# Kernel tuning notes

Hardware: AMD Instinct MI355X
Metric: run time of the kernel (lower is better)

The kernel has to match this reference:

```python
import jax, jax.numpy as jnp
import numpy as np

EPS_LN = 1e-5

def layer_norm(x, g, b):
    mu = x.mean(-1, keepdims=True)
    var = ((x - mu) ** 2).mean(-1, keepdims=True)
    return (x - mu) / jnp.sqrt(var + EPS_LN) * g + b

def spike(x):
    # MultiSpike: quantized spike activation, forward = clip(round(x), 0, 4)
    return jnp.clip(jnp.round(x), 0.0, 4.0)

def setup_inputs() -> dict:
    key = jax.random.key(0)
    ks = jax.random.split(key, 8)
    B, C, H, W = 16, 256, 56, 56
    hid = 128
    inp = {}
    inp['feature_map'] = jax.random.normal(ks[0], (B, C, H, W), jnp.float32)
    inp['audio_feature'] = jax.random.normal(ks[1], (B, 1, C), jnp.float32)
    # MINE params
    inp['w1'] = jax.random.normal(ks[2], (hid, 2 * C), jnp.float32) / np.sqrt(2 * C)
    inp['b1'] = jnp.zeros((hid,), jnp.float32)
    inp['g1'] = jnp.ones((hid,), jnp.float32)
    inp['beta1'] = jnp.zeros((hid,), jnp.float32)
    inp['w2'] = jax.random.normal(ks[3], (hid // 2, hid), jnp.float32) / np.sqrt(hid)
    inp['b2'] = jnp.zeros((hid // 2,), jnp.float32)
    inp['g2'] = jnp.ones((hid // 2,), jnp.float32)
    inp['beta2'] = jnp.zeros((hid // 2,), jnp.float32)
    inp['w3'] = jax.random.normal(ks[4], (1, hid // 2), jnp.float32) / np.sqrt(hid // 2)
    inp['b3'] = jnp.zeros((1,), jnp.float32)
    # MI params
    inp['pw'] = jax.random.normal(ks[5], (C, C), jnp.float32) / np.sqrt(C)
    inp['pb'] = jnp.zeros((C,), jnp.float32)
    inp['pg'] = jnp.ones((C,), jnp.float32)
    inp['pbeta'] = jnp.zeros((C,), jnp.float32)
    return inp

def reference(feature_map, audio_feature, w1, b1, g1, beta1, w2, b2, g2, beta2,
              w3, b3, pw, pb, pg, pbeta):
    B, C, H, W = feature_map.shape
    # visual tokens: [B*H*W, C]
    visual = feature_map.transpose(0, 2, 3, 1).reshape(B * H * W, C)
    # broadcast audio to every spatial position: [B*H*W, C]
    audio = jnp.broadcast_to(audio_feature[:, 0][:, None, None, :], (B, H, W, C)).reshape(B * H * W, C)
    # MINE MLP on joint features
    joint = jnp.concatenate([visual, audio], axis=1)            # [BHW, 2C]
    h = spike(layer_norm(joint @ w1.T + b1, g1, beta1))          # [BHW, 128]
    h = spike(layer_norm(h @ w2.T + b2, g2, beta2))              # [BHW, 64]
    mi = (h @ w3.T + b3)[:, 0]                                   # [BHW]
    mi_map = mi.reshape(B, 1, H * W)
    fm_flat = feature_map.reshape(B, C, H * W)
    # MI-weighted pooling: [B,1,C]
    x = jnp.einsum('bos,bcs->boc', mi_map, fm_flat)
    x = x @ pw.T + pb                                            # proj (dropout = eval identity)
    x = spike(layer_norm(x, pg, pbeta))                          # [B,1,C]
    fusion_map = jnp.einsum('bchw,bc->bchw', feature_map, x[:, 0])
    mi4 = mi_map.reshape(B, 1, H, W)
    mi4 = (mi4 - mi4.min()) / (mi4.max() - mi4.min() + 1e-6)     # global min-max norm
    return fusion_map, mi4
```

## Files before the change

### kernel.cpp

```cpp
#include <hip/hip_runtime.h>

#define HW 3136
#define NPOS 12845056

__device__ __forceinline__ unsigned fkey(float f) {
  unsigned u = __float_as_uint(f);
  return (u & 0x80000000u) ? ~u : (u | 0x80000000u);
}
__device__ __forceinline__ float funkey(unsigned u) {
  return __uint_as_float((u & 0x80000000u) ? (u & 0x7FFFFFFFu) : ~u);
}
__device__ __forceinline__ float spikef(float x) {
  return fminf(fmaxf(rintf(x), 0.0f), 4.0f);
}

__global__ __launch_bounds__(256) void prep_kernel(
    const float* __restrict__ audio, const float* __restrict__ w1,
    const float* __restrict__ b1, float* __restrict__ a_pre,
    float* __restrict__ pool, unsigned* __restrict__ mm)
{
  __shared__ float au[256];
  int b = blockIdx.x, t = threadIdx.x;
  au[t] = audio[b*256 + t];
  pool[b*256 + t] = 0.0f;
  if (b == 0 && t == 0) { mm[0] = 0xFFFFFFFFu; mm[1] = 0u; }
  __syncthreads();
  int w = t >> 6, l = t & 63;
  float a0 = au[l], a1 = au[l+64], a2 = au[l+128], a3 = au[l+192];
  for (int jj = 0; jj < 32; ++jj) {
    int j = w*32 + jj;
    const float* row = w1 + j*512 + 256;
    float s = row[l]*a0 + row[l+64]*a1 + row[l+128]*a2 + row[l+192]*a3;
    #pragma unroll
    for (int off = 32; off; off >>= 1) s += __shfl_xor(s, off);
    if (l == 0) a_pre[b*128 + j] = s + b1[j];
  }
}

__global__ __launch_bounds__(256) void mlp_kernel(
    const float* __restrict__ fm, const float* __restrict__ w1,
    const float* __restrict__ w2, const float* __restrict__ b2,
    const float* __restrict__ w3, const float* __restrict__ b3,
    const float* __restrict__ g1, const float* __restrict__ be1,
    const float* __restrict__ g2, const float* __restrict__ be2,
    const float* __restrict__ a_pre, float* __restrict__ mi_out,
    float* __restrict__ pool, unsigned* __restrict__ mm)
{
  __shared__ float fm_t[32][32];
  __shared__ float wAT[32][132];
  __shared__ float h1n[128][36];
  __shared__ float wB[64][33];
  __shared__ float h2n[64][36];
  __shared__ float red[8][32];
  __shared__ float red2[8][32];
  __shared__ float miL[32];

  const int b = blockIdx.y, tile = blockIdx.x;
  const int s0 = tile * 32;
  const int t = threadIdx.x;
  const int ig = t >> 5;
  const int jg = t & 31;

  const size_t fm_base = (size_t)b * 256 * HW;

  float acc[4][4] = {};
  for (int kt = 0; kt < 8; ++kt) {
    __syncthreads();
    {
      int cc = t >> 3, q = t & 7;
      const float4 v = *reinterpret_cast<const float4*>(
          fm + fm_base + (size_t)(kt*32 + cc) * HW + s0 + q*4);
      *reinterpret_cast<float4*>(&fm_t[cc][q*4]) = v;
    }
    #pragma unroll
    for (int r = 0; r < 16; ++r) {
      int idx = t + r*256; int j = idx >> 5, cc = idx & 31;
      wAT[cc][j] = w1[j*512 + kt*32 + cc];
    }
    __syncthreads();
    #pragma unroll 8
    for (int cc = 0; cc < 32; ++cc) {
      const float4 f  = *reinterpret_cast<const float4*>(&fm_t[cc][ig*4]);
      const float4 wv = *reinterpret_cast<const float4*>(&wAT[cc][jg*4]);
      float fv[4] = {f.x, f.y, f.z, f.w};
      float wvv[4] = {wv.x, wv.y, wv.z, wv.w};
      #pragma unroll
      for (int ii = 0; ii < 4; ++ii)
        #pragma unroll
        for (int jj = 0; jj < 4; ++jj)
          acc[ii][jj] += fv[ii] * wvv[jj];
    }
  }
  float ap[4];
  #pragma unroll
  for (int jj = 0; jj < 4; ++jj) ap[jj] = a_pre[b*128 + jg*4 + jj];
  #pragma unroll
  for (int jj = 0; jj < 4; ++jj)
    #pragma unroll
    for (int ii = 0; ii < 4; ++ii)
      h1n[jg*4+jj][ig*4+ii] = acc[ii][jj] + ap[jj];
  __syncthreads();

  const int i_ = t & 31, p = t >> 5;
  {
    float s = 0;
    #pragma unroll
    for (int q = 0; q < 16; ++q) s += h1n[p*16+q][i_];
    red[p][i_] = s;
  }
  __syncthreads();
  float mu = 0;
  #pragma unroll
  for (int pp = 0; pp < 8; ++pp) mu += red[pp][i_];
  mu *= (1.0f/128.0f);
  {
    float s2 = 0;
    #pragma unroll
    for (int q = 0; q < 16; ++q) { float d = h1n[p*16+q][i_] - mu; s2 += d*d; }
    red2[p][i_] = s2;
  }
  __syncthreads();
  float var = 0;
  #pragma unroll
  for (int pp = 0; pp < 8; ++pp) var += red2[pp][i_];
  var *= (1.0f/128.0f);
  float sq = sqrtf(var + 1e-5f);
  #pragma unroll
  for (int q = 0; q < 16; ++q) {
    int j = p*16 + q;
    float v = (h1n[j][i_] - mu) / sq * g1[j] + be1[j];
    h1n[j][i_] = spikef(v);
  }

  float acc2[4][2] = {};
  for (int kc = 0; kc < 4; ++kc) {
    __syncthreads();
    #pragma unroll
    for (int r = 0; r < 8; ++r) {
      int idx = t + r*256; int j2 = idx >> 5, k = idx & 31;
      wB[j2][k] = w2[j2*128 + kc*32 + k];
    }
    __syncthreads();
    #pragma unroll 8
    for (int k = 0; k < 32; ++k) {
      const float4 h = *reinterpret_cast<const float4*>(&h1n[kc*32+k][ig*4]);
      float w0 = wB[jg][k], w1v = wB[jg+32][k];
      acc2[0][0] += h.x*w0;  acc2[1][0] += h.y*w0;  acc2[2][0] += h.z*w0;  acc2[3][0] += h.w*w0;
      acc2[0][1] += h.x*w1v; acc2[1][1] += h.y*w1v; acc2[2][1] += h.z*w1v; acc2[3][1] += h.w*w1v;
    }
  }
  {
    float b2v0 = b2[jg], b2v1 = b2[jg+32];
    #pragma unroll
    for (int ii = 0; ii < 4; ++ii) {
      h2n[jg][ig*4+ii]    = acc2[ii][0] + b2v0;
      h2n[jg+32][ig*4+ii] = acc2[ii][1] + b2v1;
    }
  }
  __syncthreads();

  {
    float s = 0;
    #pragma unroll
    for (int q = 0; q < 8; ++q) s += h2n[p*8+q][i_];
    red[p][i_] = s;
  }
  __syncthreads();
  float mu2 = 0;
  #pragma unroll
  for (int pp = 0; pp < 8; ++pp) mu2 += red[pp][i_];
  mu2 *= (1.0f/64.0f);
  {
    float s2 = 0;
    #pragma unroll
    for (int q = 0; q < 8; ++q) { float d = h2n[p*8+q][i_] - mu2; s2 += d*d; }
    red2[p][i_] = s2;
  }
  __syncthreads();
  float var2 = 0;
  #pragma unroll
  for (int pp = 0; pp < 8; ++pp) var2 += red2[pp][i_];
  var2 *= (1.0f/64.0f);
  float sq2 = sqrtf(var2 + 1e-5f);
  #pragma unroll
  for (int q = 0; q < 8; ++q) {
    int j = p*8 + q;
    float v = (h2n[j][i_] - mu2) / sq2 * g2[j] + be2[j];
    h2n[j][i_] = spikef(v);
  }
  __syncthreads();

  {
    float s = 0;
    #pragma unroll
    for (int q = 0; q < 8; ++q) s += h2n[p*8+q][i_] * w3[p*8+q];
    red[p][i_] = s;
  }
  __syncthreads();
  if (t < 32) {
    float m = b3[0];
    #pragma unroll
    for (int pp = 0; pp < 8; ++pp) m += red[pp][t];
    miL[t] = m;
    mi_out[b*HW + s0 + t] = m;
    float mn = m, mx = m;
    #pragma unroll
    for (int off = 16; off; off >>= 1) {
      mn = fminf(mn, __shfl_xor(mn, off));
      mx = fmaxf(mx, __shfl_xor(mx, off));
    }
    if (t == 0) {
      atomicMin(&mm[0], fkey(mn));
      atomicMax(&mm[1], fkey(mx));
    }
  }
  __syncthreads();

  const int cg = t >> 5;
  const float miv = miL[i_];
  for (int c = cg; c < 256; c += 8) {
    float v = fm[fm_base + (size_t)c * HW + s0 + i_] * miv;
    #pragma unroll
    for (int off = 16; off; off >>= 1) v += __shfl_xor(v, off);
    if (i_ == 0) atomicAdd(&pool[b*256 + c], v);
  }
}

__global__ __launch_bounds__(256) void scale_kernel(
    const float* __restrict__ pool, const float* __restrict__ pw,
    const float* __restrict__ pb, const float* __restrict__ pg,
    const float* __restrict__ pbeta, float* __restrict__ scale,
    const unsigned* __restrict__ mm, float* __restrict__ gpar)
{
  __shared__ float pl[256];
  __shared__ float xsh[256];
  __shared__ float rs[4], rs2[4];
  int b = blockIdx.x, t = threadIdx.x;
  pl[t] = pool[b*256 + t];
  __syncthreads();
  int w = t >> 6, l = t & 63;
  float p0 = pl[l], p1 = pl[l+64], p2 = pl[l+128], p3 = pl[l+192];
  for (int jj = 0; jj < 64; ++jj) {
    int j = w*64 + jj;
    const float* row = pw + j*256;
    float s = row[l]*p0 + row[l+64]*p1 + row[l+128]*p2 + row[l+192]*p3;
    #pragma unroll
    for (int off = 32; off; off >>= 1) s += __shfl_xor(s, off);
    if (l == 0) xsh[j] = s;
  }
  __syncthreads();
  float x = xsh[t] + pb[t];
  float s = x;
  #pragma unroll
  for (int off = 32; off; off >>= 1) s += __shfl_xor(s, off);
  if (l == 0) rs[w] = s;
  __syncthreads();
  float mu = (rs[0]+rs[1]+rs[2]+rs[3]) * (1.0f/256.0f);
  float d = x - mu;
  float s2 = d*d;
  #pragma unroll
  for (int off = 32; off; off >>= 1) s2 += __shfl_xor(s2, off);
  if (l == 0) rs2[w] = s2;
  __syncthreads();
  float var = (rs2[0]+rs2[1]+rs2[2]+rs2[3]) * (1.0f/256.0f);
  float v = d / sqrtf(var + 1e-5f) * pg[t] + pbeta[t];
  scale[b*256 + t] = spikef(v);
  if (b == 0 && t == 0) {
    float mn = funkey(mm[0]), mx = funkey(mm[1]);
    gpar[0] = mn;
    gpar[1] = mx - mn + 1e-6f;
  }
}

__global__ __launch_bounds__(256) void fuse_kernel(
    const float4* __restrict__ fm4, const float* __restrict__ scale,
    const float4* __restrict__ mi4, const float* __restrict__ gpar,
    float4* __restrict__ out4, float4* __restrict__ mi4out)
{
  int bid = blockIdx.x;
  if (bid < 12544) {
    int idx = bid*256 + (int)threadIdx.x;
    int row = idx / 784;
    float s = scale[row];
    float4 v = fm4[idx];
    out4[idx] = make_float4(v.x*s, v.y*s, v.z*s, v.w*s);
  } else {
    int idx = (bid - 12544)*256 + (int)threadIdx.x;
    float gmin = gpar[0], den = gpar[1];
    float4 v = mi4[idx];
    mi4out[idx] = make_float4((v.x-gmin)/den, (v.y-gmin)/den,
                              (v.z-gmin)/den, (v.w-gmin)/den);
  }
}

extern "C" void kernel_launch(void* const* d_in, const int* in_sizes, int n_in,
                              void* d_out, int out_size, void* d_ws, size_t ws_size,
                              hipStream_t stream)
{
  const float* fm    = (const float*)d_in[0];
  const float* audio = (const float*)d_in[1];
  const float* w1    = (const float*)d_in[2];
  const float* b1    = (const float*)d_in[3];
  const float* g1    = (const float*)d_in[4];
  const float* be1   = (const float*)d_in[5];
  const float* w2    = (const float*)d_in[6];
  const float* b2    = (const float*)d_in[7];
  const float* g2    = (const float*)d_in[8];
  const float* be2   = (const float*)d_in[9];
  const float* w3    = (const float*)d_in[10];
  const float* b3    = (const float*)d_in[11];
  const float* pw    = (const float*)d_in[12];
  const float* pb    = (const float*)d_in[13];
  const float* pg    = (const float*)d_in[14];
  const float* pbeta = (const float*)d_in[15];

  float* ws    = (float*)d_ws;
  float* a_pre = ws;
  float* pool  = ws + 2048;
  float* scale = ws + 6144;
  float* mi    = ws + 10240;
  unsigned* mm = (unsigned*)(ws + 60416);
  float* gpar  = ws + 60418;

  float* out    = (float*)d_out;
  float* mi4out = out + NPOS;

  prep_kernel<<<16, 256, 0, stream>>>(audio, w1, b1, a_pre, pool, mm);
  mlp_kernel<<<dim3(98, 16), 256, 0, stream>>>(fm, w1, w2, b2, w3, b3,
                                               g1, be1, g2, be2,
                                               a_pre, mi, pool, mm);
  scale_kernel<<<16, 256, 0, stream>>>(pool, pw, pb, pg, pbeta, scale, mm, gpar);
  fuse_kernel<<<12593, 256, 0, stream>>>((const float4*)fm, scale,
                                         (const float4*)mi, gpar,
                                         (float4*)out, (float4*)mi4out);
}
```

Before: 350.5 us.

## Restructure MLP kernel to per-thread pixel register accumulation with pretransposed weights

```diff
diff --git a/kernel.cpp b/kernel.cpp
--- a/kernel.cpp
+++ b/kernel.cpp
@@ -16,213 +16,156 @@
 
 __global__ __launch_bounds__(256) void prep_kernel(
     const float* __restrict__ audio, const float* __restrict__ w1,
-    const float* __restrict__ b1, float* __restrict__ a_pre,
-    float* __restrict__ pool, unsigned* __restrict__ mm)
-{
-  __shared__ float au[256];
-  int b = blockIdx.x, t = threadIdx.x;
-  au[t] = audio[b*256 + t];
-  pool[b*256 + t] = 0.0f;
-  if (b == 0 && t == 0) { mm[0] = 0xFFFFFFFFu; mm[1] = 0u; }
-  __syncthreads();
-  int w = t >> 6, l = t & 63;
-  float a0 = au[l], a1 = au[l+64], a2 = au[l+128], a3 = au[l+192];
-  for (int jj = 0; jj < 32; ++jj) {
-    int j = w*32 + jj;
-    const float* row = w1 + j*512 + 256;
-    float s = row[l]*a0 + row[l+64]*a1 + row[l+128]*a2 + row[l+192]*a3;
-    #pragma unroll
-    for (int off = 32; off; off >>= 1) s += __shfl_xor(s, off);
-    if (l == 0) a_pre[b*128 + j] = s + b1[j];
-  }
-}
-
-__global__ __launch_bounds__(256) void mlp_kernel(
-    const float* __restrict__ fm, const float* __restrict__ w1,
-    const float* __restrict__ w2, const float* __restrict__ b2,
+    const float* __restrict__ b1, const float* __restrict__ w2,
+    float* __restrict__ a_pre, float* __restrict__ w1t,
+    float* __restrict__ w2t, float* __restrict__ pool,
+    unsigned* __restrict__ mm)
+{
+  int gid = blockIdx.x * 256 + threadIdx.x;
+  for (int idx = gid; idx < 32768; idx += 20480) {
+    int c = idx >> 7, j = idx & 127;
+    w1t[idx] = w1[j * 512 + c];
+  }
+  if (gid < 8192) {
+    int k = gid >> 6, j2 = gid & 63;
+    w2t[gid] = w2[j2 * 128 + k];
+  }
+  if (gid < 4096) pool[gid] = 0.0f;
+  if (gid == 0) { mm[0] = 0xFFFFFFFFu; mm[1] = 0u; }
+  if (gid < 2048) {
+    int b = gid >> 7, j = gid & 127;
+    const float* wr = w1 + j * 512 + 256;
+    const float* av = audio + b * 256;
+    float s = 0.f;
+    for (int c = 0; c < 256; ++c) s = fmaf(wr[c], av[c], s);
+    a_pre[gid] = s + b1[j];
+  }
+}
+
+__global__ __launch_bounds__(128) void mlp_kernel(
+    const float* __restrict__ fm, const float* __restrict__ w1t,
+    const float* __restrict__ w2t, const float* __restrict__ b2,
     const float* __restrict__ w3, const float* __restrict__ b3,
     const float* __restrict__ g1, const float* __restrict__ be1,
     const float* __restrict__ g2, const float* __restrict__ be2,
     const float* __restrict__ a_pre, float* __restrict__ mi_out,
     float* __restrict__ pool, unsigned* __restrict__ mm)
 {
-  __shared__ float fm_t[32][32];
-  __shared__ float wAT[32][132];
-  __shared__ float h1n[128][36];
-  __shared__ float wB[64][33];
-  __shared__ float h2n[64][36];
-  __shared__ float red[8][32];
-  __shared__ float red2[8][32];
-  __shared__ float miL[32];
-
-  const int b = blockIdx.y, tile = blockIdx.x;
-  const int s0 = tile * 32;
-  const int t = threadIdx.x;
-  const int ig = t >> 5;
-  const int jg = t & 31;
+  __shared__ float h1lds[128][64];
+  __shared__ float red[2][64];
+  __shared__ float red2[2][64];
+  __shared__ float milds[64];
+
+  const int b  = blockIdx.y;
+  const int s0 = blockIdx.x * 64;
+  const int t  = threadIdx.x;
+  const int l  = t & 63;
+  const int wv = __builtin_amdgcn_readfirstlane(t >> 6);
 
   const size_t fm_base = (size_t)b * 256 * HW;
-
-  float acc[4][4] = {};
-  for (int kt = 0; kt < 8; ++kt) {
-    __syncthreads();
-    {
-      int cc = t >> 3, q = t & 7;
-      const float4 v = *reinterpret_cast<const float4*>(
-          fm + fm_base + (size_t)(kt*32 + cc) * HW + s0 + q*4);
-      *reinterpret_cast<float4*>(&fm_t[cc][q*4]) = v;
-    }
-    #pragma unroll
-    for (int r = 0; r < 16; ++r) {
-      int idx = t + r*256; int j = idx >> 5, cc = idx & 31;
-      wAT[cc][j] = w1[j*512 + kt*32 + cc];
-    }
-    __syncthreads();
-    #pragma unroll 8
-    for (int cc = 0; cc < 32; ++cc) {
-      const float4 f  = *reinterpret_cast<const float4*>(&fm_t[cc][ig*4]);
-      const float4 wv = *reinterpret_cast<const float4*>(&wAT[cc][jg*4]);
-      float fv[4] = {f.x, f.y, f.z, f.w};
-      float wvv[4] = {wv.x, wv.y, wv.z, wv.w};
-      #pragma unroll
-      for (int ii = 0; ii < 4; ++ii)
-        #pragma unroll
-        for (int jj = 0; jj < 4; ++jj)
-          acc[ii][jj] += fv[ii] * wvv[jj];
-    }
-  }
-  float ap[4];
-  #pragma unroll
-  for (int jj = 0; jj < 4; ++jj) ap[jj] = a_pre[b*128 + jg*4 + jj];
-  #pragma unroll
-  for (int jj = 0; jj < 4; ++jj)
-    #pragma unroll
-    for (int ii = 0; ii < 4; ++ii)
-      h1n[jg*4+jj][ig*4+ii] = acc[ii][jj] + ap[jj];
-  __syncthreads();
-
-  const int i_ = t & 31, p = t >> 5;
+  const float* fmp = fm + fm_base + s0 + l;
+
+  float acc[64];
+  #pragma unroll
+  for (int j = 0; j < 64; ++j) acc[j] = 0.f;
+
+  float xv = fmp[0];
+  for (int c = 0; c < 256; ++c) {
+    const float* wr = w1t + c * 128 + wv * 64;
+    float xn = (c < 255) ? fmp[(size_t)(c + 1) * HW] : 0.f;
+    #pragma unroll
+    for (int j = 0; j < 64; ++j) acc[j] = fmaf(xv, wr[j], acc[j]);
+    xv = xn;
+  }
   {
-    float s = 0;
-    #pragma unroll
-    for (int q = 0; q < 16; ++q) s += h1n[p*16+q][i_];
-    red[p][i_] = s;
-  }
-  __syncthreads();
-  float mu = 0;
-  #pragma unroll
-  for (int pp = 0; pp < 8; ++pp) mu += red[pp][i_];
-  mu *= (1.0f/128.0f);
+    const float* ap = a_pre + b * 128 + wv * 64;
+    #pragma unroll
+    for (int j = 0; j < 64; ++j) acc[j] += ap[j];
+  }
+
+  float s = 0.f;
+  #pragma unroll
+  for (int j = 0; j < 64; ++j) s += acc[j];
+  red[wv][l] = s;
+  __syncthreads();
+  float mu = (red[0][l] + red[1][l]) * (1.0f / 128.0f);
+  float s2 = 0.f;
+  #pragma unroll
+  for (int j = 0; j < 64; ++j) { float d = acc[j] - mu; s2 = fmaf(d, d, s2); }
+  red2[wv][l] = s2;
+  __syncthreads();
+  float var = (red2[0][l] + red2[1][l]) * (1.0f / 128.0f);
+  float inv = 1.0f / sqrtf(var + 1e-5f);
   {
-    float s2 = 0;
-    #pragma unroll
-    for (int q = 0; q < 16; ++q) { float d = h1n[p*16+q][i_] - mu; s2 += d*d; }
-    red2[p][i_] = s2;
-  }
-  __syncthreads();
-  float var = 0;
-  #pragma unroll
-  for (int pp = 0; pp < 8; ++pp) var += red2[pp][i_];
-  var *= (1.0f/128.0f);
-  float sq = sqrtf(var + 1e-5f);
-  #pragma unroll
-  for (int q = 0; q < 16; ++q) {
-    int j = p*16 + q;
-    float v = (h1n[j][i_] - mu) / sq * g1[j] + be1[j];
-    h1n[j][i_] = spikef(v);
-  }
-
-  float acc2[4][2] = {};
-  for (int kc = 0; kc < 4; ++kc) {
-    __syncthreads();
-    #pragma unroll
-    for (int r = 0; r < 8; ++r) {
-      int idx = t + r*256; int j2 = idx >> 5, k = idx & 31;
-      wB[j2][k] = w2[j2*128 + kc*32 + k];
-    }
-    __syncthreads();
-    #pragma unroll 8
-    for (int k = 0; k < 32; ++k) {
-      const float4 h = *reinterpret_cast<const float4*>(&h1n[kc*32+k][ig*4]);
-      float w0 = wB[jg][k], w1v = wB[jg+32][k];
-      acc2[0][0] += h.x*w0;  acc2[1][0] += h.y*w0;  acc2[2][0] += h.z*w0;  acc2[3][0] += h.w*w0;
-      acc2[0][1] += h.x*w1v; acc2[1][1] += h.y*w1v; acc2[2][1] += h.z*w1v; acc2[3][1] += h.w*w1v;
-    }
-  }
-  {
-    float b2v0 = b2[jg], b2v1 = b2[jg+32];
-    #pragma unroll
-    for (int ii = 0; ii < 4; ++ii) {
-      h2n[jg][ig*4+ii]    = acc2[ii][0] + b2v0;
-      h2n[jg+32][ig*4+ii] = acc2[ii][1] + b2v1;
-    }
-  }
-  __syncthreads();
-
-  {
-    float s = 0;
-    #pragma unroll
-    for (int q = 0; q < 8; ++q) s += h2n[p*8+q][i_];
-    red[p][i_] = s;
-  }
-  __syncthreads();
-  float mu2 = 0;
-  #pragma unroll
-  for (int pp = 0; pp < 8; ++pp) mu2 += red[pp][i_];
-  mu2 *= (1.0f/64.0f);
-  {
-    float s2 = 0;
-    #pragma unroll
-    for (int q = 0; q < 8; ++q) { float d = h2n[p*8+q][i_] - mu2; s2 += d*d; }
-    red2[p][i_] = s2;
-  }
-  __syncthreads();
-  float var2 = 0;
-  #pragma unroll
-  for (int pp = 0; pp < 8; ++pp) var2 += red2[pp][i_];
-  var2 *= (1.0f/64.0f);
-  float sq2 = sqrtf(var2 + 1e-5f);
-  #pragma unroll
-  for (int q = 0; q < 8; ++q) {
-    int j = p*8 + q;
-    float v = (h2n[j][i_] - mu2) / sq2 * g2[j] + be2[j];
-    h2n[j][i_] = spikef(v);
-  }
-  __syncthreads();
-
-  {
-    float s = 0;
-    #pragma unroll
-    for (int q = 0; q < 8; ++q) s += h2n[p*8+q][i_] * w3[p*8+q];
-    red[p][i_] = s;
-  }
-  __syncthreads();
-  if (t < 32) {
-    float m = b3[0];
-    #pragma unroll
-    for (int pp = 0; pp < 8; ++pp) m += red[pp][t];
-    miL[t] = m;
-    mi_out[b*HW + s0 + t] = m;
-    float mn = m, mx = m;
-    #pragma unroll
-    for (int off = 16; off; off >>= 1) {
+    const float* g  = g1  + wv * 64;
+    const float* be = be1 + wv * 64;
+    #pragma unroll
+    for (int j = 0; j < 64; ++j)
+      h1lds[wv * 64 + j][l] = spikef((acc[j] - mu) * inv * g[j] + be[j]);
+  }
+  __syncthreads();
+
+  float acc2[64];
+  #pragma unroll
+  for (int j = 0; j < 64; ++j) acc2[j] = 0.f;
+  for (int kk = 0; kk < 64; ++kk) {
+    int k = wv * 64 + kk;
+    float xh = h1lds[k][l];
+    const float* wr = w2t + k * 64;
+    #pragma unroll
+    for (int j = 0; j < 64; ++j) acc2[j] = fmaf(xh, wr[j], acc2[j]);
+  }
+  __syncthreads();
+  float (*comb)[64] = (float(*)[64])h1lds;
+  if (wv == 1) {
+    #pragma unroll
+    for (int j = 0; j < 64; ++j) comb[j][l] = acc2[j];
+  }
+  __syncthreads();
+
+  if (wv == 0) {
+    float h2[64];
+    float sm = 0.f;
+    #pragma unroll
+    for (int j = 0; j < 64; ++j) {
+      h2[j] = acc2[j] + comb[j][l] + b2[j];
+      sm += h2[j];
+    }
+    float mu2 = sm * (1.0f / 64.0f);
+    float v2 = 0.f;
+    #pragma unroll
+    for (int j = 0; j < 64; ++j) { float d = h2[j] - mu2; v2 = fmaf(d, d, v2); }
+    float inv2 = 1.0f / sqrtf(v2 * (1.0f / 64.0f) + 1e-5f);
+    float mi = b3[0];
+    #pragma unroll
+    for (int j = 0; j < 64; ++j) {
+      float p = spikef((h2[j] - mu2) * inv2 * g2[j] + be2[j]);
+      mi = fmaf(p, w3[j], mi);
+    }
+    mi_out[b * HW + s0 + l] = mi;
+    milds[l] = mi;
+    float mn = mi, mx = mi;
+    #pragma unroll
+    for (int off = 32; off; off >>= 1) {
       mn = fminf(mn, __shfl_xor(mn, off));
       mx = fmaxf(mx, __shfl_xor(mx, off));
     }
-    if (t == 0) {
-      atomicMin(&mm[0], fkey(mn));
-      atomicMax(&mm[1], fkey(mx));
-    }
-  }
-  __syncthreads();
-
-  const int cg = t >> 5;
-  const float miv = miL[i_];
-  for (int c = cg; c < 256; c += 8) {
-    float v = fm[fm_base + (size_t)c * HW + s0 + i_] * miv;
-    #pragma unroll
-    for (int off = 16; off; off >>= 1) v += __shfl_xor(v, off);
-    if (i_ == 0) atomicAdd(&pool[b*256 + c], v);
+    if (l == 0) {
+      unsigned kmn = fkey(mn), kmx = fkey(mx);
+      volatile unsigned* vmm = (volatile unsigned*)mm;
+      if (kmn < vmm[0]) atomicMin(&mm[0], kmn);
+      if (kmx > vmm[1]) atomicMax(&mm[1], kmx);
+    }
+  }
+  __syncthreads();
+
+  float miv = milds[l];
+  for (int ci = 0; ci < 128; ++ci) {
+    int c = (wv << 7) + ci;
+    float v = fmp[(size_t)c * HW] * miv;
+    #pragma unroll
+    for (int off = 32; off; off >>= 1) v += __shfl_xor(v, off);
+    if (l == 0) atomicAdd(&pool[b * 256 + c], v);
   }
 }
 
@@ -319,14 +262,17 @@
   float* pool  = ws + 2048;
   float* scale = ws + 6144;
   float* mi    = ws + 10240;
-  unsigned* mm = (unsigned*)(ws + 60416);
-  float* gpar  = ws + 60418;
+  float* w1t   = ws + 60416;
+  float* w2t   = ws + 93184;
+  unsigned* mm = (unsigned*)(ws + 101376);
+  float* gpar  = ws + 101378;
 
   float* out    = (float*)d_out;
   float* mi4out = out + NPOS;
 
-  prep_kernel<<<16, 256, 0, stream>>>(audio, w1, b1, a_pre, pool, mm);
-  mlp_kernel<<<dim3(98, 16), 256, 0, stream>>>(fm, w1, w2, b2, w3, b3,
+  prep_kernel<<<80, 256, 0, stream>>>(audio, w1, b1, w2, a_pre, w1t, w2t,
+                                      pool, mm);
+  mlp_kernel<<<dim3(49, 16), 128, 0, stream>>>(fm, w1t, w2t, b2, w3, b3,
                                                g1, be1, g2, be2,
                                                a_pre, mi, pool, mm);
   scale_kernel<<<16, 256, 0, stream>>>(pool, pw, pb, pg, pbeta, scale, mm, gpar);
```

Measured after the change: 437.1 us. 24.7% more time.
